# Performance work log

Measured on AMD Instinct MI355X. Metric: run time of the kernel, lower is better.

## Reference

```python
import jax, jax.numpy as jnp
import numpy as np

EMPTY, TRUE, FALSE = 0.0, 1.0, 2.0  # MemoryVal ternary encoding

B = 2048          # batch
IN_BITS = 4096    # raw input bits
N_IN, N_ST, N_OUT = 2048, 1024, 1024
K = 14            # bits (connections) per neuron -> memory_size = 2**K
M = 2 ** K


def setup_inputs() -> dict:
    key = jax.random.key(0)
    ks = jax.random.split(key, 8)
    return {
        "input_bits": jax.random.randint(ks[0], (B, IN_BITS), 0, 2, dtype=jnp.int32),
        "state_bits": jax.random.randint(ks[1], (B, N_ST), 0, 2, dtype=jnp.int32),
        "in_conn": jax.random.randint(ks[2], (N_IN, K), 0, IN_BITS, dtype=jnp.int32),
        "in_mem": jax.random.randint(ks[3], (N_IN, M), 0, 3).astype(jnp.float32),
        "st_conn": jax.random.randint(ks[4], (N_ST, K), 0, N_IN + N_ST, dtype=jnp.int32),
        "st_mem": jax.random.randint(ks[5], (N_ST, M), 0, 3).astype(jnp.float32),
        "out_conn": jax.random.randint(ks[6], (N_OUT, K), 0, N_IN + N_ST, dtype=jnp.int32),
        "out_mem": jax.random.randint(ks[7], (N_OUT, M), 0, 3).astype(jnp.float32),
    }


def _ram_layer(bits, conn, mem):
    """bits: [B, T] 0/1; conn: [N, K] indices into T; mem: [N, 2**K] ternary."""
    k = conn.shape[1]
    g = bits[:, conn].astype(jnp.int32)                      # [B, N, K] gathered local bits
    w = (2 ** jnp.arange(k - 1, -1, -1)).astype(jnp.int32)   # MSB-first packing (matches _get_desired_bits)
    addr = jnp.sum(g * w, axis=-1)                           # [B, N] memory addresses
    vals = mem[jnp.arange(mem.shape[0])[None, :], addr]      # [B, N] per-neuron LUT lookup
    return jnp.where(vals == TRUE, 1.0, 0.0).astype(jnp.float32)  # neuron fires iff TRUE


def reference(input_bits, state_bits, in_conn, in_mem, st_conn, st_mem, out_conn, out_mem):
    h_in = _ram_layer(input_bits, in_conn, in_mem)                          # [B, N_IN]
    s_inp = jnp.concatenate([h_in, state_bits.astype(h_in.dtype)], axis=1)  # [B, N_IN+N_ST]
    s_out = _ram_layer(s_inp, st_conn, st_mem)                              # [B, N_ST]
    o_inp = jnp.concatenate([h_in, s_out], axis=1)                          # [B, N_IN+N_ST]
    return _ram_layer(o_inp, out_conn, out_mem)                             # [B, N_OUT]
```

## Files before the change

kernel.cpp:

```cpp
#include <hip/hip_runtime.h>
#include <stdint.h>

#define BATCH   2048
#define KBITS   14
#define MW      512
#define BROW    128
#define PAD     129

#define IM_F 33554432L
#define SM_F 16777216L

#define W_IN  4096
#define W_ST  5120
#define W_END 37888

__global__ __launch_bounds__(256) void pack_all(
    const int4* __restrict__ in_b, const int4* __restrict__ st_b,
    const float4* __restrict__ im, const float4* __restrict__ sm,
    const float4* __restrict__ om,
    uint32_t* __restrict__ bits1, uint32_t* __restrict__ buf,
    uint32_t* __restrict__ tbl) {
    const int gw = (blockIdx.x * 256 + threadIdx.x) >> 6;
    const int lane = threadIdx.x & 63;
    uint32_t nib[8];
    long wbase;
    if (gw < W_ST) {
        const int4* src;
        long ebase;
        if (gw < W_IN) { src = in_b; ebase = (long)gw << 11; }
        else           { src = st_b; ebase = (long)(gw - W_IN) << 11; }
        const int4* p = src + (ebase >> 2) + lane;
        int4 r[8];
#pragma unroll
        for (int j = 0; j < 8; j++) r[j] = p[j * 64];
#pragma unroll
        for (int j = 0; j < 8; j++)
            nib[j] = (uint32_t)(r[j].x == 1) | ((uint32_t)(r[j].y == 1) << 1) |
                     ((uint32_t)(r[j].z == 1) << 2) | ((uint32_t)(r[j].w == 1) << 3);
        wbase = ebase >> 5;
    } else {
        long fbase = (long)(gw - W_ST) << 11;
        const float4* src;
        long eb;
        if (fbase < IM_F)             { src = im; eb = fbase; }
        else if (fbase < IM_F + SM_F) { src = sm; eb = fbase - IM_F; }
        else                          { src = om; eb = fbase - IM_F - SM_F; }
        const float4* p = src + (eb >> 2) + lane;
        float4 r[8];
#pragma unroll
        for (int j = 0; j < 8; j++) r[j] = p[j * 64];
#pragma unroll
        for (int j = 0; j < 8; j++)
            nib[j] = (uint32_t)(r[j].x == 1.0f) | ((uint32_t)(r[j].y == 1.0f) << 1) |
                     ((uint32_t)(r[j].z == 1.0f) << 2) | ((uint32_t)(r[j].w == 1.0f) << 3);
        wbase = fbase >> 5;
    }
    uint32_t w[8];
#pragma unroll
    for (int j = 0; j < 8; j++) {
        uint32_t x = nib[j] << (4 * (lane & 7));
        x |= __shfl_xor(x, 1, 64);
        x |= __shfl_xor(x, 2, 64);
        x |= __shfl_xor(x, 4, 64);
        w[j] = x;
    }
    if ((lane & 7) == 0) {
        const int s = lane >> 3;
        if (gw < W_IN) {
#pragma unroll
            for (int j = 0; j < 8; j++) bits1[wbase + j * 8 + s] = w[j];
        } else if (gw < W_ST) {
#pragma unroll
            for (int j = 0; j < 8; j++) {
                long g = wbase + j * 8 + s;
                buf[(g >> 5) * BROW + 64 + (g & 31)] = w[j];
            }
        } else {
#pragma unroll
            for (int j = 0; j < 8; j++) tbl[wbase + j * 8 + s] = w[j];
        }
    }
}

template <int NW, int MODE>
__global__ __launch_bounds__(256) void ram_layer(const uint32_t* __restrict__ src,
                                                 const int* __restrict__ conn,
                                                 const uint32_t* __restrict__ memp,
                                                 uint32_t* __restrict__ dst,
                                                 float* __restrict__ fout) {
    __shared__ uint32_t lds[64 * PAD];
    const int tid = threadIdx.x;
    const int b0 = blockIdx.y * 64;
    {
        const uint4* g = (const uint4*)(src + (long)b0 * BROW);
        for (int v = tid; v < 64 * BROW / 4; v += 256) {
            uint4 d = g[v];
            int row = v >> 5;
            int col = (v & 31) * 4;
            uint32_t* p = lds + row * PAD + col;
            p[0] = d.x; p[1] = d.y; p[2] = d.z; p[3] = d.w;
        }
    }
    __syncthreads();

    const int lane = tid & 63;
    const int wv = __builtin_amdgcn_readfirstlane(tid >> 6);
    const int n0 = blockIdx.x * (4 * NW) + wv * NW;
    const uint32_t* myrow = lds + lane * PAD;

    unsigned long long msk = 0;
#pragma unroll 2
    for (int i = 0; i < NW; ++i) {
        const int n = n0 + i;
        const int* c = conn + n * KBITS;
        uint32_t addr = 0;
#pragma unroll
        for (int k = 0; k < KBITS; k++) {
            int idx = c[k];
            int wd = idx >> 5;
            if (MODE == 2 && idx >= 2048) wd += 32;
            addr = (addr << 1) | ((myrow[wd] >> (idx & 31)) & 1u);
        }
        uint32_t v = memp[(long)n * MW + (addr >> 5)];
        unsigned long long m = __ballot(((v >> (addr & 31)) & 1u) != 0);
        msk = (lane == i) ? m : msk;
    }

    unsigned long long x = msk;
#define TSTEP(S, M)                                                         \
    {                                                                       \
        unsigned long long t =                                              \
            (unsigned long long)__shfl_xor((long long)x, S, 64);            \
        x = (lane & S) ? ((x & ~(M)) | ((t & ~(M)) >> S))                   \
                       : ((x & (M)) | ((t & (M)) << S));                    \
    }
    TSTEP(32, 0x00000000ffffffffULL)
    TSTEP(16, 0x0000ffff0000ffffULL)
    TSTEP(8,  0x00ff00ff00ff00ffULL)
    TSTEP(4,  0x0f0f0f0f0f0f0f0fULL)
    TSTEP(2,  0x3333333333333333ULL)
    TSTEP(1,  0x5555555555555555ULL)
#undef TSTEP

    if (MODE == 0) {
        ((uint16_t*)(dst + (long)(b0 + lane) * BROW))[n0 >> 4] = (uint16_t)x;
    } else if (MODE == 1) {
        ((uint8_t*)(dst + (long)(b0 + lane) * BROW + 96))[n0 >> 3] = (uint8_t)x;
    } else {
        float* o = fout + (long)(b0 + lane) * 1024 + n0;
        float4 f0, f1;
        f0.x = (float)((x >> 0) & 1); f0.y = (float)((x >> 1) & 1);
        f0.z = (float)((x >> 2) & 1); f0.w = (float)((x >> 3) & 1);
        f1.x = (float)((x >> 4) & 1); f1.y = (float)((x >> 5) & 1);
        f1.z = (float)((x >> 6) & 1); f1.w = (float)((x >> 7) & 1);
        ((float4*)o)[0] = f0;
        ((float4*)o)[1] = f1;
    }
}

extern "C" void kernel_launch(void* const* d_in, const int* in_sizes, int n_in,
                              void* d_out, int out_size, void* d_ws, size_t ws_size,
                              hipStream_t stream) {
    const int*   input_bits = (const int*)d_in[0];
    const int*   state_bits = (const int*)d_in[1];
    const int*   in_conn    = (const int*)d_in[2];
    const float* in_mem     = (const float*)d_in[3];
    const int*   st_conn    = (const int*)d_in[4];
    const float* st_mem     = (const float*)d_in[5];
    const int*   out_conn   = (const int*)d_in[6];
    const float* out_mem    = (const float*)d_in[7];
    float*       out        = (float*)d_out;

    char* ws = (char*)d_ws;
    uint32_t* bits1 = (uint32_t*)(ws);
    uint32_t* buf   = (uint32_t*)(ws + 1048576);
    uint32_t* tbl   = (uint32_t*)(ws + 2097152);
    uint32_t* im_p  = tbl;
    uint32_t* sm_p  = tbl + 1048576;
    uint32_t* om_p  = tbl + 1572864;

    pack_all<<<W_END / 4, 256, 0, stream>>>(
        (const int4*)input_bits, (const int4*)state_bits,
        (const float4*)in_mem, (const float4*)st_mem, (const float4*)out_mem,
        bits1, buf, tbl);

    ram_layer<16, 0><<<dim3(32, 32), 256, 0, stream>>>(bits1, in_conn, im_p, buf, nullptr);
    ram_layer<8, 1><<<dim3(32, 32), 256, 0, stream>>>(buf, st_conn, sm_p, buf, nullptr);
    ram_layer<8, 2><<<dim3(32, 32), 256, 0, stream>>>(buf, out_conn, om_p, nullptr, out);
}
```

Measured before the change: 350.5 us.

## Pack LUTs and input bits with per-lane strided layout, drop shuffles

```diff
diff --git a/kernel.cpp b/kernel.cpp
--- a/kernel.cpp
+++ b/kernel.cpp
@@ -9,56 +9,68 @@
 
 #define IM_F 33554432L
 #define SM_F 16777216L
-
-#define W_IN  4096
-#define W_ST  5120
-#define W_END 37888
-
-__global__ __launch_bounds__(256) void pack_all(
-    const int4* __restrict__ in_b, const int4* __restrict__ st_b,
-    const float4* __restrict__ im, const float4* __restrict__ sm,
-    const float4* __restrict__ om,
-    uint32_t* __restrict__ bits1, uint32_t* __restrict__ buf,
-    uint32_t* __restrict__ tbl) {
+#define OM_F 16777216L
+
+__global__ __launch_bounds__(256) void pack_mem(const float4* __restrict__ im,
+                                                const float4* __restrict__ sm,
+                                                const float4* __restrict__ om,
+                                                uint32_t* __restrict__ tbl) {
     const int gw = (blockIdx.x * 256 + threadIdx.x) >> 6;
     const int lane = threadIdx.x & 63;
-    uint32_t nib[8];
-    long wbase;
-    if (gw < W_ST) {
-        const int4* src;
-        long ebase;
-        if (gw < W_IN) { src = in_b; ebase = (long)gw << 11; }
-        else           { src = st_b; ebase = (long)(gw - W_IN) << 11; }
-        const int4* p = src + (ebase >> 2) + lane;
-        int4 r[8];
-#pragma unroll
-        for (int j = 0; j < 8; j++) r[j] = p[j * 64];
-#pragma unroll
-        for (int j = 0; j < 8; j++)
-            nib[j] = (uint32_t)(r[j].x == 1) | ((uint32_t)(r[j].y == 1) << 1) |
-                     ((uint32_t)(r[j].z == 1) << 2) | ((uint32_t)(r[j].w == 1) << 3);
-        wbase = ebase >> 5;
-    } else {
-        long fbase = (long)(gw - W_ST) << 11;
-        const float4* src;
-        long eb;
-        if (fbase < IM_F)             { src = im; eb = fbase; }
-        else if (fbase < IM_F + SM_F) { src = sm; eb = fbase - IM_F; }
-        else                          { src = om; eb = fbase - IM_F - SM_F; }
-        const float4* p = src + (eb >> 2) + lane;
-        float4 r[8];
-#pragma unroll
-        for (int j = 0; j < 8; j++) r[j] = p[j * 64];
-#pragma unroll
-        for (int j = 0; j < 8; j++)
-            nib[j] = (uint32_t)(r[j].x == 1.0f) | ((uint32_t)(r[j].y == 1.0f) << 1) |
-                     ((uint32_t)(r[j].z == 1.0f) << 2) | ((uint32_t)(r[j].w == 1.0f) << 3);
-        wbase = fbase >> 5;
-    }
+    const long f0 = (long)gw << 11;
+    const float4* src;
+    long eb;
+    if (f0 < IM_F)              { src = im; eb = f0; }
+    else if (f0 < IM_F + SM_F)  { src = sm; eb = f0 - IM_F; }
+    else                        { src = om; eb = f0 - IM_F - SM_F; }
+    const float4* p = src + (eb >> 2) + lane;
+    float4 r[8];
+#pragma unroll
+    for (int j = 0; j < 8; j++) r[j] = p[j * 64];
+    uint32_t w = 0;
+#pragma unroll
+    for (int j = 0; j < 8; j++) {
+        uint32_t nib = (uint32_t)(r[j].x == 1.0f) | ((uint32_t)(r[j].y == 1.0f) << 1) |
+                       ((uint32_t)(r[j].z == 1.0f) << 2) | ((uint32_t)(r[j].w == 1.0f) << 3);
+        w |= nib << (4 * j);
+    }
+    tbl[(f0 >> 5) + lane] = w;
+}
+
+__global__ __launch_bounds__(256) void pack_in(const int4* __restrict__ src,
+                                               uint32_t* __restrict__ bits1) {
+    const int gw = (blockIdx.x * 256 + threadIdx.x) >> 6;
+    const int lane = threadIdx.x & 63;
+    const long f0 = (long)gw << 11;
+    const int4* p = src + (f0 >> 2) + lane;
+    int4 r[8];
+#pragma unroll
+    for (int j = 0; j < 8; j++) r[j] = p[j * 64];
+    uint32_t w = 0;
+#pragma unroll
+    for (int j = 0; j < 8; j++) {
+        uint32_t nib = (uint32_t)(r[j].x == 1) | ((uint32_t)(r[j].y == 1) << 1) |
+                       ((uint32_t)(r[j].z == 1) << 2) | ((uint32_t)(r[j].w == 1) << 3);
+        w |= nib << (4 * j);
+    }
+    bits1[(f0 >> 5) + lane] = w;
+}
+
+__global__ __launch_bounds__(256) void pack_st(const int4* __restrict__ src,
+                                               uint32_t* __restrict__ buf) {
+    const int gw = (blockIdx.x * 256 + threadIdx.x) >> 6;
+    const int lane = threadIdx.x & 63;
+    const long ebase = (long)gw << 11;
+    const int4* p = src + (ebase >> 2) + lane;
+    int4 r[8];
+#pragma unroll
+    for (int j = 0; j < 8; j++) r[j] = p[j * 64];
     uint32_t w[8];
 #pragma unroll
     for (int j = 0; j < 8; j++) {
-        uint32_t x = nib[j] << (4 * (lane & 7));
+        uint32_t nib = (uint32_t)(r[j].x == 1) | ((uint32_t)(r[j].y == 1) << 1) |
+                       ((uint32_t)(r[j].z == 1) << 2) | ((uint32_t)(r[j].w == 1) << 3);
+        uint32_t x = nib << (4 * (lane & 7));
         x |= __shfl_xor(x, 1, 64);
         x |= __shfl_xor(x, 2, 64);
         x |= __shfl_xor(x, 4, 64);
@@ -66,18 +78,11 @@
     }
     if ((lane & 7) == 0) {
         const int s = lane >> 3;
-        if (gw < W_IN) {
-#pragma unroll
-            for (int j = 0; j < 8; j++) bits1[wbase + j * 8 + s] = w[j];
-        } else if (gw < W_ST) {
-#pragma unroll
-            for (int j = 0; j < 8; j++) {
-                long g = wbase + j * 8 + s;
-                buf[(g >> 5) * BROW + 64 + (g & 31)] = w[j];
-            }
-        } else {
-#pragma unroll
-            for (int j = 0; j < 8; j++) tbl[wbase + j * 8 + s] = w[j];
+        const long wbase = ebase >> 5;
+#pragma unroll
+        for (int j = 0; j < 8; j++) {
+            long g = wbase + j * 8 + s;
+            buf[(g >> 5) * BROW + 64 + (g & 31)] = w[j];
         }
     }
 }
@@ -117,12 +122,21 @@
 #pragma unroll
         for (int k = 0; k < KBITS; k++) {
             int idx = c[k];
-            int wd = idx >> 5;
-            if (MODE == 2 && idx >= 2048) wd += 32;
-            addr = (addr << 1) | ((myrow[wd] >> (idx & 31)) & 1u);
+            int wd, bit;
+            if (MODE == 0) {
+                wd = ((idx >> 11) << 6) | ((idx >> 2) & 63);
+                bit = (((idx >> 8) & 7) << 2) | (idx & 3);
+            } else {
+                wd = idx >> 5;
+                if (MODE == 2 && idx >= 2048) wd += 32;
+                bit = idx & 31;
+            }
+            addr = (addr << 1) | ((myrow[wd] >> bit) & 1u);
         }
-        uint32_t v = memp[(long)n * MW + (addr >> 5)];
-        unsigned long long m = __ballot(((v >> (addr & 31)) & 1u) != 0);
+        uint32_t word = ((addr >> 11) << 6) | ((addr >> 2) & 63);
+        uint32_t bit = (((addr >> 8) & 7) << 2) | (addr & 3);
+        uint32_t v = memp[(long)n * MW + word];
+        unsigned long long m = __ballot(((v >> bit) & 1u) != 0);
         msk = (lane == i) ? m : msk;
     }
 
@@ -179,10 +193,10 @@
     uint32_t* sm_p  = tbl + 1048576;
     uint32_t* om_p  = tbl + 1572864;
 
-    pack_all<<<W_END / 4, 256, 0, stream>>>(
-        (const int4*)input_bits, (const int4*)state_bits,
-        (const float4*)in_mem, (const float4*)st_mem, (const float4*)out_mem,
-        bits1, buf, tbl);
+    pack_in <<<1024, 256, 0, stream>>>((const int4*)input_bits, bits1);
+    pack_st <<<256,  256, 0, stream>>>((const int4*)state_bits, buf);
+    pack_mem<<<8192, 256, 0, stream>>>((const float4*)in_mem, (const float4*)st_mem,
+                                       (const float4*)out_mem, tbl);
 
     ram_layer<16, 0><<<dim3(32, 32), 256, 0, stream>>>(bits1, in_conn, im_p, buf, nullptr);
     ram_layer<8, 1><<<dim3(32, 32), 256, 0, stream>>>(buf, st_conn, sm_p, buf, nullptr);
```

Measured after the change: 361.9 us. +3.3%, slower.
